# Optimization experiments

Measured on AMD Instinct MI355X. Metric: run time of the kernel, lower is better.

The kernel has to match this reference:

```python
import jax, jax.numpy as jnp
import numpy as np

N_DIM = 16
E_DIM = 16
M_DIM = 16
HIDDEN = 64
N_EDGE = 1_600_000
N_NODE = 100_000


def setup_inputs() -> dict:
    key = jax.random.key(0)
    k1, k2, k3, k4, k5, k6, k7 = jax.random.split(key, 7)
    index_v = jax.random.randint(k1, (N_EDGE,), 0, N_NODE, dtype=jnp.int32)
    h_w = jax.random.normal(k2, (N_EDGE, N_DIM), dtype=jnp.float32)
    e_vw = jax.random.normal(k3, (N_EDGE, E_DIM), dtype=jnp.float32)
    # NNet params: Linear(e_dim, hidden) -> ReLU -> Linear(hidden, n_dim*m_dim)
    s1 = 1.0 / np.sqrt(E_DIM)
    s2 = 1.0 / np.sqrt(HIDDEN)
    W1 = jax.random.uniform(k4, (E_DIM, HIDDEN), jnp.float32, -s1, s1)
    b1 = jax.random.uniform(k5, (HIDDEN,), jnp.float32, -s1, s1)
    W2 = jax.random.uniform(k6, (HIDDEN, N_DIM * M_DIM), jnp.float32, -s2, s2)
    b2 = jax.random.uniform(k7, (N_DIM * M_DIM,), jnp.float32, -s2, s2)
    return {"index_v": index_v, "h_w": h_w, "e_vw": e_vw, "n_node": N_NODE,
            "W1": W1, "b1": b1, "W2": W2, "b2": b2}


def reference(index_v, h_w, e_vw, n_node, W1, b1, W2, b2):
    # Edge MLP: [n_edge, e_dim] -> [n_edge, n_dim*m_dim]
    hid = jax.nn.relu(e_vw @ W1 + b1)
    A_vw = (hid @ W2 + b2).reshape(-1, M_DIM, N_DIM)  # [n_edge, m_dim, n_dim]
    # Per-edge matvec: bmm(A_vw, h_w[:, :, None]) -> [n_edge, m_dim]
    m_vw = jnp.einsum("emn,en->em", A_vw, h_w)
    # Scatter-add messages to target nodes: [n_node, m_dim]
    m_v = jax.ops.segment_sum(m_vw, index_v, num_segments=n_node)
    return m_v
```

## Files before the change

kernel.cpp:

```cpp
#include <hip/hip_runtime.h>
#include <stdint.h>

typedef __bf16 bf16x8 __attribute__((ext_vector_type(8)));
typedef float  f32x4  __attribute__((ext_vector_type(4)));
typedef float  fvec4  __attribute__((ext_vector_type(4)));
typedef float  f32x2  __attribute__((ext_vector_type(2)));

#define EDIM   16
#define HIDDEN 64
#define MDIM   16
#define NDIM   16
#define KCHUNKS 32
#define NREP   8
#define WPB    8

__device__ __forceinline__ uint32_t pack_trunc(float x, float y) {
    return __builtin_amdgcn_perm(__builtin_bit_cast(uint32_t, x),
                                 __builtin_bit_cast(uint32_t, y),
                                 0x03020706u);
}

__device__ __forceinline__ uint16_t f32_to_bf16_rne(float f) {
    uint32_t u = __builtin_bit_cast(uint32_t, f);
    u += 0x7FFFu + ((u >> 16) & 1u);
    return (uint16_t)(u >> 16);
}

__device__ __forceinline__ bf16x8 u4_as_bf16x8(uint32_t a, uint32_t b,
                                               uint32_t c, uint32_t d) {
    union { uint32_t u[4]; bf16x8 v; } x;
    x.u[0] = a; x.u[1] = b; x.u[2] = c; x.u[3] = d;
    return x.v;
}

__device__ __forceinline__ f32x2 pk_mul(f32x2 a, f32x2 b) {
    f32x2 d;
    asm("v_pk_mul_f32 %0, %1, %2" : "=v"(d) : "v"(a), "v"(b));
    return d;
}

__device__ __forceinline__ void atomic_add_s(const float* base, uint32_t off,
                                             float v) {
    asm volatile("global_atomic_add_f32 %0, %1, %2"
                 :: "v"(off), "v"(v), "s"(base) : "memory");
}

__device__ __forceinline__ void load_eh(const float* p, uint32_t ro,
                                        fvec4& a, fvec4& b) {
    const fvec4* pp = (const fvec4*)(p + ro);
    a = __builtin_nontemporal_load(pp);
    b = __builtin_nontemporal_load(pp + 1);
}

__device__ __forceinline__ int4 load_idx4(const int* __restrict__ idx,
                                          int r, int n_edge, bool full) {
    int4 v;
    if (full) {
        v.x = __builtin_nontemporal_load(idx + r + 0);
        v.y = __builtin_nontemporal_load(idx + r + 1);
        v.z = __builtin_nontemporal_load(idx + r + 2);
        v.w = __builtin_nontemporal_load(idx + r + 3);
    } else {
        v.x = __builtin_nontemporal_load(idx + min(r + 0, n_edge - 1));
        v.y = __builtin_nontemporal_load(idx + min(r + 1, n_edge - 1));
        v.z = __builtin_nontemporal_load(idx + min(r + 2, n_edge - 1));
        v.w = __builtin_nontemporal_load(idx + min(r + 3, n_edge - 1));
    }
    return v;
}

__device__ __forceinline__ void hid_stage(fvec4 ea, fvec4 eb, int q,
                                          const bf16x8* w1f, ushort* hidWr) {
    uint32_t au0 = pack_trunc(ea.x, ea.y);
    uint32_t au1 = pack_trunc(ea.z, ea.w);
    uint32_t au2 = pack_trunc(eb.x, eb.y);
    uint32_t au3 = pack_trunc(eb.z, eb.w);
    if (q == 2) { au0 = 0x00003F80u; au1 = au2 = au3 = 0; }
    else if (q == 3) { au0 = au1 = au2 = au3 = 0; }
    bf16x8 av = u4_as_bf16x8(au0, au1, au2, au3);
    #pragma unroll
    for (int nt = 0; nt < 4; nt++) {
        f32x4 hc = {0.f, 0.f, 0.f, 0.f};
        hc = __builtin_amdgcn_mfma_f32_16x16x32_bf16(av, w1f[nt], hc, 0, 0, 0);
        uint32_t lo = pack_trunc(fmaxf(hc[0], 0.f), fmaxf(hc[1], 0.f));
        uint32_t hi = pack_trunc(fmaxf(hc[2], 0.f), fmaxf(hc[3], 0.f));
        *(uint2*)(hidWr + nt * 256) = make_uint2(lo, hi);
    }
}

__global__ __launch_bounds__(512, 4) void msg_mfma32(
    const int*   __restrict__ idx,
    const float* __restrict__ h_w,
    const float* __restrict__ e_vw,
    const float* __restrict__ W1,
    const float* __restrict__ b1,
    const float* __restrict__ W2,
    const float* __restrict__ b2,
    float*       __restrict__ outb,
    int n_edge, int rep_stride)
{
    __align__(16) __shared__ ushort sB[KCHUNKS * 512];
    __align__(16) __shared__ ushort sHid[WPB * 2 * 1024];

    const int tid = threadIdx.x;

    const int xcd = __builtin_amdgcn_s_getreg(6164) & (NREP - 1);
    const float* out = outb + (size_t)xcd * (size_t)rep_stride;

    for (int t = tid; t < KCHUNKS * 512; t += 512) {
        int c = t >> 9, r = t & 511;
        int qq = r >> 7, m = (r >> 3) & 15, j = r & 7;
        int k = 2 * c + (qq >> 1);
        int n = ((qq & 1) << 3) + j;
        sB[t] = f32_to_bf16_rne(W2[k * 256 + m * 16 + n]);
    }

    const int lane = tid & 63;
    const int q    = lane >> 4;
    const int col  = lane & 15;
    const int w    = tid >> 6;

    uint32_t w1u[4][4];
    #pragma unroll
    for (int nt = 0; nt < 4; nt++) {
        #pragma unroll
        for (int d = 0; d < 4; d++) w1u[nt][d] = 0;
        #pragma unroll
        for (int j = 0; j < 8; j++) {
            int k = q * 8 + j;
            float v = 0.f;
            if (k < 16)       v = W1[k * 64 + nt * 16 + col];
            else if (k == 16) v = b1[nt * 16 + col];
            w1u[nt][j >> 1] |= ((uint32_t)f32_to_bf16_rne(v)) << ((j & 1) * 16);
        }
    }

    uint32_t b2u[4] = {0, 0, 0, 0};
    if (q < 2) {
        const float* bp = b2 + col * 16 + q * 8;
        #pragma unroll
        for (int j = 0; j < 8; j++)
            b2u[j >> 1] |= ((uint32_t)f32_to_bf16_rne(bp[j])) << ((j & 1) * 16);
    }
    __syncthreads();

    bf16x8 w1f[4];
    #pragma unroll
    for (int nt = 0; nt < 4; nt++)
        w1f[nt] = u4_as_bf16x8(w1u[nt][0], w1u[nt][1], w1u[nt][2], w1u[nt][3]);
    const bf16x8 b2f = u4_as_bf16x8(b2u[0], b2u[1], b2u[2], b2u[3]);

    const int nhalf = (q & 1) << 3;
    const int ntile = (n_edge + 31) >> 5;
    const int wave_id = blockIdx.x * WPB + w;
    const int wstride = gridDim.x * WPB;
    if (wave_id >= ntile) return;

    const ushort* hidRd0 = &sHid[(w * 2 + 0) * 1024 + (q >> 1) * 16 + col];
    const ushort* hidRd1 = hidRd0 + 1024;
    ushort*       hidWr0 = &sHid[(w * 2 + 0) * 1024 + col * 16 + q * 4];
    ushort*       hidWr1 = hidWr0 + 1024;
    const ushort* bRd    = &sB[q * 128 + col * 8];
    const uint32_t col4  = (uint32_t)col * 4u;

    int t = wave_id;
    fvec4 e0, e1, e2, e3, h0, h1, h2, h3; int4 nd0, nd1; bool full;
    {
        int rbase = t * 32;
        full = (rbase + 32 <= n_edge);
        int row0 = full ? (rbase + col)      : min(rbase + col,      n_edge - 1);
        int row1 = full ? (rbase + 16 + col) : min(rbase + 16 + col, n_edge - 1);
        uint32_t ro0 = (uint32_t)row0 * 16u + (uint32_t)nhalf;
        uint32_t ro1 = (uint32_t)row1 * 16u + (uint32_t)nhalf;
        load_eh(e_vw, ro0, e0, e1);
        load_eh(e_vw, ro1, e2, e3);
        load_eh(h_w,  ro0, h0, h1);
        load_eh(h_w,  ro1, h2, h3);
        nd0 = load_idx4(idx, rbase + q * 4,      n_edge, full);
        nd1 = load_idx4(idx, rbase + 16 + q * 4, n_edge, full);
    }

    while (true) {
        int tn = t + wstride;
        bool have_next = (tn < ntile);

        hid_stage(e0, e1, q, w1f, hidWr0);
        hid_stage(e2, e3, q, w1f, hidWr1);

        bool nfull = false;
        if (have_next) {
            int rbase = tn * 32;
            nfull = (rbase + 32 <= n_edge);
            int row0 = nfull ? (rbase + col)      : min(rbase + col,      n_edge - 1);
            int row1 = nfull ? (rbase + 16 + col) : min(rbase + 16 + col, n_edge - 1);
            load_eh(e_vw, (uint32_t)row0 * 16u + (uint32_t)nhalf, e0, e1);
            load_eh(e_vw, (uint32_t)row1 * 16u + (uint32_t)nhalf, e2, e3);
        }

        f32x2 hp0; hp0.x = h0.x; hp0.y = h0.y;
        f32x2 hp1; hp1.x = h0.z; hp1.y = h0.w;
        f32x2 hp2; hp2.x = h1.x; hp2.y = h1.y;
        f32x2 hp3; hp3.x = h1.z; hp3.y = h1.w;
        f32x2 hq0; hq0.x = h2.x; hq0.y = h2.y;
        f32x2 hq1; hq1.x = h2.z; hq1.y = h2.w;
        f32x2 hq2; hq2.x = h3.x; hq2.y = h3.y;
        f32x2 hq3; hq3.x = h3.z; hq3.y = h3.w;

        f32x4 acc0 = {0.f, 0.f, 0.f, 0.f};
        f32x4 acc1 = {0.f, 0.f, 0.f, 0.f};
        {
            bf16x8 af0 = u4_as_bf16x8(pack_trunc(hp0.x, hp0.y), pack_trunc(hp1.x, hp1.y),
                                      pack_trunc(hp2.x, hp2.y), pack_trunc(hp3.x, hp3.y));
            acc0 = __builtin_amdgcn_mfma_f32_16x16x32_bf16(af0, b2f, acc0, 0, 0, 0);
            bf16x8 af1 = u4_as_bf16x8(pack_trunc(hq0.x, hq0.y), pack_trunc(hq1.x, hq1.y),
                                      pack_trunc(hq2.x, hq2.y), pack_trunc(hq3.x, hq3.y));
            acc1 = __builtin_amdgcn_mfma_f32_16x16x32_bf16(af1, b2f, acc1, 0, 0, 0);
        }

        #pragma unroll
        for (int c = 0; c < KCHUNKS; c++) {
            bf16x8 bfb = *(const bf16x8*)(bRd + c * 512);
            {
                uint32_t hku = ((uint32_t)hidRd0[c * 32]) << 16;
                float hkf = __builtin_bit_cast(float, hku);
                f32x2 hk2; hk2.x = hkf; hk2.y = hkf;
                f32x2 p0 = pk_mul(hk2, hp0);
                f32x2 p1 = pk_mul(hk2, hp1);
                f32x2 p2 = pk_mul(hk2, hp2);
                f32x2 p3 = pk_mul(hk2, hp3);
                bf16x8 af = u4_as_bf16x8(pack_trunc(p0.x, p0.y), pack_trunc(p1.x, p1.y),
                                         pack_trunc(p2.x, p2.y), pack_trunc(p3.x, p3.y));
                acc0 = __builtin_amdgcn_mfma_f32_16x16x32_bf16(af, bfb, acc0, 0, 0, 0);
            }
            {
                uint32_t hku = ((uint32_t)hidRd1[c * 32]) << 16;
                float hkf = __builtin_bit_cast(float, hku);
                f32x2 hk2; hk2.x = hkf; hk2.y = hkf;
                f32x2 p0 = pk_mul(hk2, hq0);
                f32x2 p1 = pk_mul(hk2, hq1);
                f32x2 p2 = pk_mul(hk2, hq2);
                f32x2 p3 = pk_mul(hk2, hq3);
                bf16x8 af = u4_as_bf16x8(pack_trunc(p0.x, p0.y), pack_trunc(p1.x, p1.y),
                                         pack_trunc(p2.x, p2.y), pack_trunc(p3.x, p3.y));
                acc1 = __builtin_amdgcn_mfma_f32_16x16x32_bf16(af, bfb, acc1, 0, 0, 0);
            }
        }

        int4 ndn0, ndn1;
        if (have_next) {
            int rbase = tn * 32;
            int row0 = nfull ? (rbase + col)      : min(rbase + col,      n_edge - 1);
            int row1 = nfull ? (rbase + 16 + col) : min(rbase + 16 + col, n_edge - 1);
            load_eh(h_w, (uint32_t)row0 * 16u + (uint32_t)nhalf, h0, h1);
            load_eh(h_w, (uint32_t)row1 * 16u + (uint32_t)nhalf, h2, h3);
            ndn0 = load_idx4(idx, rbase + q * 4,      n_edge, nfull);
            ndn1 = load_idx4(idx, rbase + 16 + q * 4, n_edge, nfull);
        }

        if (full) {
            atomic_add_s(out, (uint32_t)nd0.x * 64u + col4, acc0[0]);
            atomic_add_s(out, (uint32_t)nd0.y * 64u + col4, acc0[1]);
            atomic_add_s(out, (uint32_t)nd0.z * 64u + col4, acc0[2]);
            atomic_add_s(out, (uint32_t)nd0.w * 64u + col4, acc0[3]);
            atomic_add_s(out, (uint32_t)nd1.x * 64u + col4, acc1[0]);
            atomic_add_s(out, (uint32_t)nd1.y * 64u + col4, acc1[1]);
            atomic_add_s(out, (uint32_t)nd1.z * 64u + col4, acc1[2]);
            atomic_add_s(out, (uint32_t)nd1.w * 64u + col4, acc1[3]);
        } else {
            int r0 = t * 32 + q * 4;
            int r1 = r0 + 16;
            if (r0 + 0 < n_edge) atomic_add_s(out, (uint32_t)nd0.x * 64u + col4, acc0[0]);
            if (r0 + 1 < n_edge) atomic_add_s(out, (uint32_t)nd0.y * 64u + col4, acc0[1]);
            if (r0 + 2 < n_edge) atomic_add_s(out, (uint32_t)nd0.z * 64u + col4, acc0[2]);
            if (r0 + 3 < n_edge) atomic_add_s(out, (uint32_t)nd0.w * 64u + col4, acc0[3]);
            if (r1 + 0 < n_edge) atomic_add_s(out, (uint32_t)nd1.x * 64u + col4, acc1[0]);
            if (r1 + 1 < n_edge) atomic_add_s(out, (uint32_t)nd1.y * 64u + col4, acc1[1]);
            if (r1 + 2 < n_edge) atomic_add_s(out, (uint32_t)nd1.z * 64u + col4, acc1[2]);
            if (r1 + 3 < n_edge) atomic_add_s(out, (uint32_t)nd1.w * 64u + col4, acc1[3]);
        }

        if (!have_next) break;
        t = tn; full = nfull; nd0 = ndn0; nd1 = ndn1;
    }
}

__global__ __launch_bounds__(512, 6) void msg_mfma_legacy(
    const int*   __restrict__ idx,
    const float* __restrict__ h_w,
    const float* __restrict__ e_vw,
    const float* __restrict__ W1,
    const float* __restrict__ b1,
    const float* __restrict__ W2,
    const float* __restrict__ b2,
    float*       __restrict__ out,
    int n_edge)
{
    __align__(16) __shared__ ushort sB[KCHUNKS * 512];
    __align__(16) __shared__ ushort sHid[WPB * 64 * 16];
    const int tid = threadIdx.x;
    for (int t = tid; t < KCHUNKS * 512; t += 512) {
        int c = t >> 9, r = t & 511;
        int qq = r >> 7, m = (r >> 3) & 15, j = r & 7;
        int k = 2 * c + (qq >> 1);
        int n = ((qq & 1) << 3) + j;
        sB[t] = f32_to_bf16_rne(W2[k * 256 + m * 16 + n]);
    }
    const int lane = tid & 63, q = lane >> 4, col = lane & 15, w = tid >> 6;
    uint32_t w1u[4][4];
    #pragma unroll
    for (int nt = 0; nt < 4; nt++) {
        #pragma unroll
        for (int d = 0; d < 4; d++) w1u[nt][d] = 0;
        #pragma unroll
        for (int j = 0; j < 8; j++) {
            int k = q * 8 + j;
            float v = 0.f;
            if (k < 16)       v = W1[k * 64 + nt * 16 + col];
            else if (k == 16) v = b1[nt * 16 + col];
            w1u[nt][j >> 1] |= ((uint32_t)f32_to_bf16_rne(v)) << ((j & 1) * 16);
        }
    }
    uint32_t b2u[4] = {0, 0, 0, 0};
    if (q < 2) {
        const float* bp = b2 + col * 16 + q * 8;
        #pragma unroll
        for (int j = 0; j < 8; j++)
            b2u[j >> 1] |= ((uint32_t)f32_to_bf16_rne(bp[j])) << ((j & 1) * 16);
    }
    __syncthreads();
    bf16x8 w1f[4];
    #pragma unroll
    for (int nt = 0; nt < 4; nt++)
        w1f[nt] = u4_as_bf16x8(w1u[nt][0], w1u[nt][1], w1u[nt][2], w1u[nt][3]);
    const bf16x8 b2f = u4_as_bf16x8(b2u[0], b2u[1], b2u[2], b2u[3]);
    const int nhalf = (q & 1) << 3;
    const int ntile = (n_edge + 15) >> 4;
    int t = blockIdx.x * WPB + w;
    const int wstride = gridDim.x * WPB;
    const ushort* hidRd = &sHid[w * 1024 + (q >> 1) * 16 + col];
    ushort*       hidWr = &sHid[w * 1024 + col * 16 + q * 4];
    const ushort* bRd   = &sB[q * 128 + col * 8];
    for (; t < ntile; t += wstride) {
        int row = min(t * 16 + col, n_edge - 1);
        const fvec4* ep = (const fvec4*)(e_vw + (size_t)row * 16 + nhalf);
        fvec4 e0 = ep[0], e1 = ep[1];
        const fvec4* hpp = (const fvec4*)(h_w + (size_t)row * 16 + nhalf);
        fvec4 h0 = hpp[0], h1 = hpp[1];
        int r0 = t * 16 + q * 4;
        int4 nd;
        nd.x = idx[min(r0 + 0, n_edge - 1)];
        nd.y = idx[min(r0 + 1, n_edge - 1)];
        nd.z = idx[min(r0 + 2, n_edge - 1)];
        nd.w = idx[min(r0 + 3, n_edge - 1)];
        hid_stage(e0, e1, q, w1f, hidWr);
        float hf[8] = {h0.x, h0.y, h0.z, h0.w, h1.x, h1.y, h1.z, h1.w};
        f32x4 acc = {0.f, 0.f, 0.f, 0.f};
        {
            uint32_t a0 = pack_trunc(hf[0], hf[1]);
            uint32_t a1 = pack_trunc(hf[2], hf[3]);
            uint32_t a2 = pack_trunc(hf[4], hf[5]);
            uint32_t a3 = pack_trunc(hf[6], hf[7]);
            acc = __builtin_amdgcn_mfma_f32_16x16x32_bf16(
                u4_as_bf16x8(a0, a1, a2, a3), b2f, acc, 0, 0, 0);
        }
        #pragma unroll
        for (int c = 0; c < KCHUNKS; c++) {
            uint32_t hku = ((uint32_t)hidRd[c * 32]) << 16;
            float hk = __builtin_bit_cast(float, hku);
            uint32_t a0 = pack_trunc(hk * hf[0], hk * hf[1]);
            uint32_t a1 = pack_trunc(hk * hf[2], hk * hf[3]);
            uint32_t a2 = pack_trunc(hk * hf[4], hk * hf[5]);
            uint32_t a3 = pack_trunc(hk * hf[6], hk * hf[7]);
            bf16x8 bfb = *(const bf16x8*)(bRd + c * 512);
            acc = __builtin_amdgcn_mfma_f32_16x16x32_bf16(
                u4_as_bf16x8(a0, a1, a2, a3), bfb, acc, 0, 0, 0);
        }
        if (r0 + 0 < n_edge) atomicAdd(out + (size_t)nd.x * 16 + col, acc[0]);
        if (r0 + 1 < n_edge) atomicAdd(out + (size_t)nd.y * 16 + col, acc[1]);
        if (r0 + 2 < n_edge) atomicAdd(out + (size_t)nd.z * 16 + col, acc[2]);
        if (r0 + 3 < n_edge) atomicAdd(out + (size_t)nd.w * 16 + col, acc[3]);
    }
}

__global__ void merge_rep(const fvec4* __restrict__ rep,
                          fvec4* __restrict__ out, int n4, int stride4)
{
    int i = blockIdx.x * blockDim.x + threadIdx.x;
    if (i >= n4) return;
    fvec4 s = rep[i];
    #pragma unroll
    for (int r = 1; r < NREP; r++)
        s += rep[(size_t)r * stride4 + i];
    out[i] = s;
}

extern "C" void kernel_launch(void* const* d_in, const int* in_sizes, int n_in,
                              void* d_out, int out_size, void* d_ws, size_t ws_size,
                              hipStream_t stream) {
    const int*   idx  = (const int*)  d_in[0];
    const float* h_w  = (const float*)d_in[1];
    const float* e_vw = (const float*)d_in[2];
    const float* W1   = (const float*)d_in[4];
    const float* b1   = (const float*)d_in[5];
    const float* W2   = (const float*)d_in[6];
    const float* b2   = (const float*)d_in[7];
    float* out = (float*)d_out;
    const int n_edge = in_sizes[0];

    const size_t out_floats = (size_t)out_size;
    const size_t need = (size_t)NREP * out_floats * sizeof(float);

    if (ws_size >= need && (out_floats & 3) == 0) {
        float* rep = (float*)d_ws;
        hipMemsetAsync(rep, 0, need, stream);
        msg_mfma32<<<1024, 512, 0, stream>>>(idx, h_w, e_vw, W1, b1, W2, b2,
                                             rep, n_edge, (int)out_floats);
        const int n4 = (int)(out_floats >> 2);
        const int mblocks = (n4 + 255) / 256;
        merge_rep<<<mblocks, 256, 0, stream>>>((const fvec4*)rep, (fvec4*)out,
                                               n4, n4);
    } else {
        hipMemsetAsync(out, 0, out_floats * sizeof(float), stream);
        msg_mfma_legacy<<<1536, 512, 0, stream>>>(idx, h_w, e_vw, W1, b1, W2,
                                                  b2, out, n_edge);
    }
}
```

Baseline: 320.6 us.

## Use op_sel broadcast pk_mul, vector index loads, and halve grid size

Replaces the manual scalar broadcast before v_pk_mul_f32 with an op_sel_hi modifier, so the hidden scalar no longer has to be duplicated into both halves of a register pair. Full-tile index loads become one 128-bit vector load instead of four scalar loads. The main kernel grid drops from 1024 to 512 blocks, so each wave handles more tiles in its persistent loop. That may lower scheduling overhead but could reduce latency hiding and occupancy.

Result: no change. 314.4 us (-1.9%).

```diff
diff --git a/kernel.cpp b/kernel.cpp
--- a/kernel.cpp
+++ b/kernel.cpp
@@ -5,6 +5,7 @@
 typedef float  f32x4  __attribute__((ext_vector_type(4)));
 typedef float  fvec4  __attribute__((ext_vector_type(4)));
 typedef float  f32x2  __attribute__((ext_vector_type(2)));
+typedef int    i32x4  __attribute__((ext_vector_type(4)));
 
 #define EDIM   16
 #define HIDDEN 64
@@ -33,9 +34,9 @@
     return x.v;
 }
 
-__device__ __forceinline__ f32x2 pk_mul(f32x2 a, f32x2 b) {
+__device__ __forceinline__ f32x2 pk_mul_bcast(f32x2 a, f32x2 b) {
     f32x2 d;
-    asm("v_pk_mul_f32 %0, %1, %2" : "=v"(d) : "v"(a), "v"(b));
+    asm("v_pk_mul_f32 %0, %1, %2 op_sel_hi:[0,1]" : "=v"(d) : "v"(a), "v"(b));
     return d;
 }
 
@@ -52,14 +53,11 @@
     b = __builtin_nontemporal_load(pp + 1);
 }
 
-__device__ __forceinline__ int4 load_idx4(const int* __restrict__ idx,
-                                          int r, int n_edge, bool full) {
-    int4 v;
+__device__ __forceinline__ i32x4 load_idx4(const int* __restrict__ idx,
+                                           int r, int n_edge, bool full) {
+    i32x4 v;
     if (full) {
-        v.x = __builtin_nontemporal_load(idx + r + 0);
-        v.y = __builtin_nontemporal_load(idx + r + 1);
-        v.z = __builtin_nontemporal_load(idx + r + 2);
-        v.w = __builtin_nontemporal_load(idx + r + 3);
+        v = __builtin_nontemporal_load((const i32x4*)(idx + r));
     } else {
         v.x = __builtin_nontemporal_load(idx + min(r + 0, n_edge - 1));
         v.y = __builtin_nontemporal_load(idx + min(r + 1, n_edge - 1));
@@ -164,7 +162,7 @@
     const uint32_t col4  = (uint32_t)col * 4u;
 
     int t = wave_id;
-    fvec4 e0, e1, e2, e3, h0, h1, h2, h3; int4 nd0, nd1; bool full;
+    fvec4 e0, e1, e2, e3, h0, h1, h2, h3; i32x4 nd0, nd1; bool full;
     {
         int rbase = t * 32;
         full = (rbase + 32 <= n_edge);
@@ -217,36 +215,35 @@
             acc1 = __builtin_amdgcn_mfma_f32_16x16x32_bf16(af1, b2f, acc1, 0, 0, 0);
         }
 
+        f32x2 hkA = {0.f, 0.f}, hkB = {0.f, 0.f};
         #pragma unroll
         for (int c = 0; c < KCHUNKS; c++) {
             bf16x8 bfb = *(const bf16x8*)(bRd + c * 512);
             {
-                uint32_t hku = ((uint32_t)hidRd0[c * 32]) << 16;
-                float hkf = __builtin_bit_cast(float, hku);
-                f32x2 hk2; hk2.x = hkf; hk2.y = hkf;
-                f32x2 p0 = pk_mul(hk2, hp0);
-                f32x2 p1 = pk_mul(hk2, hp1);
-                f32x2 p2 = pk_mul(hk2, hp2);
-                f32x2 p3 = pk_mul(hk2, hp3);
+                hkA[0] = __builtin_bit_cast(float,
+                             ((uint32_t)hidRd0[c * 32]) << 16);
+                f32x2 p0 = pk_mul_bcast(hkA, hp0);
+                f32x2 p1 = pk_mul_bcast(hkA, hp1);
+                f32x2 p2 = pk_mul_bcast(hkA, hp2);
+                f32x2 p3 = pk_mul_bcast(hkA, hp3);
                 bf16x8 af = u4_as_bf16x8(pack_trunc(p0.x, p0.y), pack_trunc(p1.x, p1.y),
                                          pack_trunc(p2.x, p2.y), pack_trunc(p3.x, p3.y));
                 acc0 = __builtin_amdgcn_mfma_f32_16x16x32_bf16(af, bfb, acc0, 0, 0, 0);
             }
             {
-                uint32_t hku = ((uint32_t)hidRd1[c * 32]) << 16;
-                float hkf = __builtin_bit_cast(float, hku);
-                f32x2 hk2; hk2.x = hkf; hk2.y = hkf;
-                f32x2 p0 = pk_mul(hk2, hq0);
-                f32x2 p1 = pk_mul(hk2, hq1);
-                f32x2 p2 = pk_mul(hk2, hq2);
-                f32x2 p3 = pk_mul(hk2, hq3);
+                hkB[0] = __builtin_bit_cast(float,
+                             ((uint32_t)hidRd1[c * 32]) << 16);
+                f32x2 p0 = pk_mul_bcast(hkB, hq0);
+                f32x2 p1 = pk_mul_bcast(hkB, hq1);
+                f32x2 p2 = pk_mul_bcast(hkB, hq2);
+                f32x2 p3 = pk_mul_bcast(hkB, hq3);
                 bf16x8 af = u4_as_bf16x8(pack_trunc(p0.x, p0.y), pack_trunc(p1.x, p1.y),
                                          pack_trunc(p2.x, p2.y), pack_trunc(p3.x, p3.y));
                 acc1 = __builtin_amdgcn_mfma_f32_16x16x32_bf16(af, bfb, acc1, 0, 0, 0);
             }
         }
 
-        int4 ndn0, ndn1;
+        i32x4 ndn0, ndn1;
         if (have_next) {
             int rbase = tn * 32;
             int row0 = nfull ? (rbase + col)      : min(rbase + col,      n_edge - 1);
@@ -412,15 +409,15 @@
 
     if (ws_size >= need && (out_floats & 3) == 0) {
         float* rep = (float*)d_ws;
-        hipMemsetAsync(rep, 0, need, stream);
-        msg_mfma32<<<1024, 512, 0, stream>>>(idx, h_w, e_vw, W1, b1, W2, b2,
-                                             rep, n_edge, (int)out_floats);
+        (void)hipMemsetAsync(rep, 0, need, stream);
+        msg_mfma32<<<512, 512, 0, stream>>>(idx, h_w, e_vw, W1, b1, W2, b2,
+                                            rep, n_edge, (int)out_floats);
         const int n4 = (int)(out_floats >> 2);
         const int mblocks = (n4 + 255) / 256;
         merge_rep<<<mblocks, 256, 0, stream>>>((const fvec4*)rep, (fvec4*)out,
                                                n4, n4);
     } else {
-        hipMemsetAsync(out, 0, out_floats * sizeof(float), stream);
+        (void)hipMemsetAsync(out, 0, out_floats * sizeof(float), stream);
         msg_mfma_legacy<<<1536, 512, 0, stream>>>(idx, h_w, e_vw, W1, b1, W2,
                                                   b2, out, n_edge);
     }
```
